# Optimization experiments

Hardware: AMD Instinct MI355X
Metric: run time of the kernel (lower is better)

Reference implementation:

```python
import jax, jax.numpy as jnp
import numpy as np

B, N, C, H, E, K = 2, 2048, 1024, 4096, 8, 2
TAU = 1.0


def setup_inputs() -> dict:
    key = jax.random.key(0)
    ks = jax.random.split(key, 9)
    x = jax.random.normal(ks[0], (B, N, C), dtype=jnp.float32)
    T = B * N
    u = jax.random.uniform(ks[1], (T, E), minval=1e-6, maxval=1.0 - 1e-6)
    gumbel_noise = -jnp.log(-jnp.log(u))  # Gumbel(0,1) samples
    s = 0.02
    gate_w = jax.random.normal(ks[2], (C, E), dtype=jnp.float32) * s
    gate_b = jnp.zeros((E,), dtype=jnp.float32)
    w1 = jax.random.normal(ks[3], (E, C, H), dtype=jnp.float32) * s
    b1 = jnp.zeros((E, H), dtype=jnp.float32)
    w2 = jax.random.normal(ks[4], (E, H, C), dtype=jnp.float32) * s
    b2 = jnp.zeros((E, C), dtype=jnp.float32)
    return {"x": x, "gumbel_noise": gumbel_noise, "gate_w": gate_w,
            "gate_b": gate_b, "w1": w1, "b1": b1, "w2": w2, "b2": b2}


def reference(x, gumbel_noise, gate_w, gate_b, w1, b1, w2, b2):
    Bb, Nn, Cc = x.shape
    x_flat = x.reshape(-1, Cc)                                  # [T, C]
    logits = x_flat @ gate_w + gate_b                           # [T, E]
    # F.gumbel_softmax(hard=False, tau=1): softmax((logits + g)/tau)
    gates = jax.nn.softmax((logits + gumbel_noise) / TAU, axis=-1)
    mean_gates = gates.mean(axis=0)
    load_balance_loss = jnp.sum(mean_gates * jnp.log(mean_gates + 1e-8))
    topk_vals, topk_idxs = jax.lax.top_k(gates, K)              # [T, K]
    T = x_flat.shape[0]
    # scatter top-k gate weights into a dense [T, E] combine matrix
    comb = jnp.zeros((T, E), dtype=gates.dtype)
    comb = comb.at[jnp.arange(T)[:, None], topk_idxs].set(topk_vals)
    # dense per-expert MLP over all tokens, then weighted combine
    h = jnp.einsum('tc,ech->teh', x_flat, w1) + b1              # [T, E, H]
    h = jax.nn.gelu(h, approximate=False)                        # exact GELU (nn.GELU)
    y = jnp.einsum('teh,ehc->tec', h, w2) + b2                  # [T, E, C]
    out = jnp.einsum('te,tec->tc', comb, y)                     # [T, C]
    return out.reshape(Bb, Nn, Cc), load_balance_loss
```

## Files before the change

### kernel.cpp

```cpp
#include <hip/hip_runtime.h>
#include <math.h>

#define TT  4096
#define CC  1024
#define HH  4096
#define EE  8
#define TKN 8192

typedef _Float16 f16x8 __attribute__((ext_vector_type(8)));
typedef float    f32x4 __attribute__((ext_vector_type(4)));

#define GLD_LDS16(g, l)                                                        \
    __builtin_amdgcn_global_load_lds(                                          \
        (const __attribute__((address_space(1))) void*)(g),                    \
        (__attribute__((address_space(3))) void*)(l), 16, 0, 0)

#define BOUNDARY(N)                                                            \
    do {                                                                       \
        asm volatile("s_waitcnt vmcnt(" #N ")" ::: "memory");                  \
        __builtin_amdgcn_s_barrier();                                          \
    } while (0)

__global__ __launch_bounds__(256) void gate_kernel(
    const float* __restrict__ x, const float* __restrict__ gn,
    const float* __restrict__ gw, const float* __restrict__ gb,
    int* __restrict__ topk_idx, float* __restrict__ topk_w,
    int* __restrict__ counts, float* __restrict__ gsum)
{
    int wave = threadIdx.x >> 6, lane = threadIdx.x & 63;
    int t = blockIdx.x * 4 + wave;
    const float* xrow = x + (size_t)t * CC;

    double acc[EE];
#pragma unroll
    for (int e = 0; e < EE; e++) acc[e] = 0.0;

#pragma unroll
    for (int i = 0; i < CC / 64; i++) {
        int c = i * 64 + lane;
        float xv = xrow[c];
        const float4* g4 = reinterpret_cast<const float4*>(gw + (size_t)c * EE);
        float4 g0 = g4[0], g1 = g4[1];
        double xd = (double)xv;
        acc[0] += xd * (double)g0.x; acc[1] += xd * (double)g0.y;
        acc[2] += xd * (double)g0.z; acc[3] += xd * (double)g0.w;
        acc[4] += xd * (double)g1.x; acc[5] += xd * (double)g1.y;
        acc[6] += xd * (double)g1.z; acc[7] += xd * (double)g1.w;
    }
#pragma unroll
    for (int e = 0; e < EE; e++)
#pragma unroll
        for (int off = 32; off > 0; off >>= 1)
            acc[e] += __shfl_xor(acc[e], off);

    double z[EE], m = -1e300;
#pragma unroll
    for (int e = 0; e < EE; e++) {
        z[e] = acc[e] + (double)gb[e] + (double)gn[(size_t)t * EE + e];
        m = fmax(m, z[e]);
    }
    double p[EE], s = 0.0;
#pragma unroll
    for (int e = 0; e < EE; e++) { p[e] = exp(z[e] - m); s += p[e]; }
    double inv = 1.0 / s;
    double g[EE];
#pragma unroll
    for (int e = 0; e < EE; e++) g[e] = p[e] * inv;

    int i1 = 0; double v1 = g[0];
#pragma unroll
    for (int e = 1; e < EE; e++) if (g[e] > v1) { v1 = g[e]; i1 = e; }
    int i2 = -1; double v2 = -1.0;
#pragma unroll
    for (int e = 0; e < EE; e++) if (e != i1 && g[e] > v2) { v2 = g[e]; i2 = e; }

    if (lane == 0) {
        topk_idx[t * 2 + 0] = i1; topk_w[t * 2 + 0] = (float)v1;
        topk_idx[t * 2 + 1] = i2; topk_w[t * 2 + 1] = (float)v2;
        atomicAdd(&counts[i1], 1);
        atomicAdd(&counts[i2], 1);
    }

    __shared__ float gp[4][EE];
    if (lane == 0) {
#pragma unroll
        for (int e = 0; e < EE; e++) gp[wave][e] = (float)g[e];
    }
    __syncthreads();
    if (threadIdx.x < EE) {
        float s4 = gp[0][threadIdx.x] + gp[1][threadIdx.x] +
                   gp[2][threadIdx.x] + gp[3][threadIdx.x];
        atomicAdd(&gsum[threadIdx.x], s4);
    }
}

__global__ __launch_bounds__(256) void transpose_f16_kernel(
    const float* __restrict__ src, _Float16* __restrict__ dst, int R, int Ccols)
{
    __shared__ float tile[64][65];
    int e = blockIdx.z;
    const float* s = src + (size_t)e * R * Ccols;
    _Float16* d = dst + (size_t)e * R * Ccols;
    int c0 = blockIdx.x * 64, r0 = blockIdx.y * 64;
    int tid = threadIdx.x;

    int lr = tid >> 4;
    int lc = (tid & 15) * 4;
#pragma unroll
    for (int i = 0; i < 4; i++) {
        int r = lr + i * 16;
        float4 v = *reinterpret_cast<const float4*>(
            s + (size_t)(r0 + r) * Ccols + c0 + lc);
        tile[r][lc + 0] = v.x; tile[r][lc + 1] = v.y;
        tile[r][lc + 2] = v.z; tile[r][lc + 3] = v.w;
    }
    __syncthreads();

    int oc = tid >> 2;
    int orr = (tid & 3) * 16;
    f16x8 o0, o1;
#pragma unroll
    for (int j = 0; j < 8; j++) o0[j] = (_Float16)tile[orr + j][oc];
#pragma unroll
    for (int j = 0; j < 8; j++) o1[j] = (_Float16)tile[orr + 8 + j][oc];
    *reinterpret_cast<f16x8*>(d + (size_t)(c0 + oc) * R + r0 + orr)     = o0;
    *reinterpret_cast<f16x8*>(d + (size_t)(c0 + oc) * R + r0 + orr + 8) = o1;
}

__global__ void scan_kernel(const int* __restrict__ counts, int* __restrict__ offsets,
                            const float* __restrict__ gsum, float* __restrict__ loss_out)
{
    if (threadIdx.x == 0) {
        int o = 0;
#pragma unroll
        for (int e = 0; e < EE; e++) { offsets[e] = o; o += counts[e]; }
        offsets[EE] = o;
        float L = 0.f;
#pragma unroll
        for (int e = 0; e < EE; e++) {
            float me = gsum[e] / (float)TT;
            L += me * logf(me + 1e-8f);
        }
        *loss_out = L;
    }
}

__global__ __launch_bounds__(256) void scatter_kernel(
    const int* __restrict__ topk_idx, const int* __restrict__ offsets,
    int* __restrict__ fill, int* __restrict__ rowtok, int* __restrict__ posmap)
{
    int t = blockIdx.x * 256 + threadIdx.x;
#pragma unroll
    for (int k = 0; k < 2; k++) {
        int e = topk_idx[t * 2 + k];
        int pos = offsets[e] + atomicAdd(&fill[e], 1);
        rowtok[pos] = t;
        posmap[t * 2 + k] = pos;
    }
}

__global__ __launch_bounds__(256) void gather_kernel(
    const float* __restrict__ x, const int* __restrict__ rowtok,
    _Float16* __restrict__ xg)
{
    int p = blockIdx.x * 2 + (threadIdx.x >> 7);
    int c = (threadIdx.x & 127) * 8;
    int t = rowtok[p];
    const float4* s = reinterpret_cast<const float4*>(x + (size_t)t * CC + c);
    float4 v0 = s[0], v1 = s[1];
    f16x8 o;
    o[0] = (_Float16)v0.x; o[1] = (_Float16)v0.y;
    o[2] = (_Float16)v0.z; o[3] = (_Float16)v0.w;
    o[4] = (_Float16)v1.x; o[5] = (_Float16)v1.y;
    o[6] = (_Float16)v1.z; o[7] = (_Float16)v1.w;
    *reinterpret_cast<f16x8*>(xg + (size_t)p * CC + c) = o;
}

__global__ __launch_bounds__(512, 2) void gemm1_kernel(
    const _Float16* __restrict__ xg, const _Float16* __restrict__ w1t,
    const float* __restrict__ b1, const int* __restrict__ offsets,
    _Float16* __restrict__ h)
{
    int GX = gridDim.x, GY = gridDim.y;
    int nwg = GX * GY * (int)gridDim.z;
    int f = blockIdx.x + GX * (blockIdx.y + GY * blockIdx.z);
    int cpx = nwg >> 3;
    f = (f & 7) * cpx + (f >> 3);
    int bx = f % GX; int tq = f / GX; int by = tq % GY; int bz = tq / GY;

    int e = bz;
    int segs = offsets[e];
    int M = offsets[e + 1] - segs;
    int m0 = bx * 256;
    if (m0 >= M) return;
    int n0 = by * 256;

    __shared__ __align__(16) _Float16 As[4][256 * 32];
    __shared__ __align__(16) _Float16 Bs[4][256 * 32];
    _Float16* AsF = &As[0][0];
    _Float16* BsF = &Bs[0][0];

    int tid = threadIdx.x;
    int wave = tid >> 6, lane = tid & 63;
    int wm = (wave >> 2) * 128, wn = (wave & 3) * 64;
    int lrow = lane & 15, kg = lane >> 4;
    int aoff = (wm + lrow) * 32 + kg * 8;
    int boff = (wn + lrow) * 32 + kg * 8;

    const _Float16* wB = w1t + (size_t)e * HH * CC;

    int r0c = tid >> 2, cc = tid & 3;
    int rmA0 = m0 + r0c;       if (rmA0 >= M) rmA0 = M - 1;
    int rmA1 = m0 + 128 + r0c; if (rmA1 >= M) rmA1 = M - 1;
    const _Float16* ap0 = xg + (size_t)(segs + rmA0) * CC + cc * 8;
    const _Float16* ap1 = xg + (size_t)(segs + rmA1) * CC + cc * 8;
    const _Float16* bp0 = wB + (size_t)(n0 + r0c) * CC + cc * 8;
    const _Float16* bp1 = wB + (size_t)(n0 + 128 + r0c) * CC + cc * 8;
    int c0 = tid * 8;

    f32x4 acc[8][4];
#pragma unroll
    for (int i = 0; i < 8; i++)
#pragma unroll
        for (int j = 0; j < 4; j++)
#pragma unroll
            for (int r = 0; r < 4; r++) acc[i][j][r] = 0.f;

    auto STAGE = [&](int nb) {
        _Float16* ad = AsF + nb * (256 * 32);
        _Float16* bd = BsF + nb * (256 * 32);
        GLD_LDS16(ap0, ad + c0);
        GLD_LDS16(ap1, ad + 4096 + c0);
        GLD_LDS16(bp0, bd + c0);
        GLD_LDS16(bp1, bd + 4096 + c0);
        ap0 += 32; ap1 += 32; bp0 += 32; bp1 += 32;
    };

    auto TILE = [&](int t, bool stage) {
        const _Float16* Ab = AsF + (t & 3) * (256 * 32) + aoff;
        const _Float16* Bb = BsF + (t & 3) * (256 * 32) + boff;
        if (stage) STAGE((t + 3) & 3);
        f16x8 aF[4], bF[4];
#pragma unroll
        for (int j = 0; j < 4; j++)
            bF[j] = *reinterpret_cast<const f16x8*>(Bb + j * 512);
#pragma unroll
        for (int i = 0; i < 4; i++)
            aF[i] = *reinterpret_cast<const f16x8*>(Ab + i * 512);
        __builtin_amdgcn_s_setprio(1);
#pragma unroll
        for (int i = 0; i < 4; i++)
#pragma unroll
            for (int j = 0; j < 4; j++)
                acc[i][j] = __builtin_amdgcn_mfma_f32_16x16x32_f16(
                    aF[i], bF[j], acc[i][j], 0, 0, 0);
        __builtin_amdgcn_s_setprio(0);
#pragma unroll
        for (int i = 0; i < 4; i++)
            aF[i] = *reinterpret_cast<const f16x8*>(Ab + (4 + i) * 512);
        __builtin_amdgcn_s_setprio(1);
#pragma unroll
        for (int i = 0; i < 4; i++)
#pragma unroll
            for (int j = 0; j < 4; j++)
                acc[4 + i][j] = __builtin_amdgcn_mfma_f32_16x16x32_f16(
                    aF[i], bF[j], acc[4 + i][j], 0, 0, 0);
        __builtin_amdgcn_s_setprio(0);
    };

    const int NK = CC / 32;
    STAGE(0); STAGE(1); STAGE(2);
    BOUNDARY(8);
    for (int t = 0; t <= NK - 4; ++t) {
        TILE(t, true);
        BOUNDARY(8);
    }
    TILE(NK - 3, false); BOUNDARY(4);
    TILE(NK - 2, false); BOUNDARY(0);
    TILE(NK - 1, false);

    int rbase = (lane >> 4) * 4;
#pragma unroll
    for (int mi = 0; mi < 8; mi++) {
#pragma unroll
        for (int ni = 0; ni < 4; ni++) {
            int gcol = n0 + wn + ni * 16 + lrow;
            float bias = b1[(size_t)e * HH + gcol];
#pragma unroll
            for (int r = 0; r < 4; r++) {
                int rowl = m0 + wm + mi * 16 + rbase + r;
                if (rowl < M) {
                    float v = acc[mi][ni][r] + bias;
                    v = 0.5f * v * (1.0f + erff(v * 0.70710678118654752f));
                    h[(size_t)(segs + rowl) * HH + gcol] = (_Float16)v;
                }
            }
        }
    }
}

__global__ __launch_bounds__(512, 2) void gemm2_kernel(
    const _Float16* __restrict__ h, const _Float16* __restrict__ w2t,
    const float* __restrict__ b2, const int* __restrict__ offsets,
    float* __restrict__ y)
{
    int GX = gridDim.x, GY = gridDim.y;
    int nwg = GX * GY * (int)gridDim.z;
    int f = blockIdx.x + GX * (blockIdx.y + GY * blockIdx.z);
    int cpx = nwg >> 3;
    f = (f & 7) * cpx + (f >> 3);
    int bx = f % GX; int tq = f / GX; int by = tq % GY; int bz = tq / GY;

    int e = bz;
    int segs = offsets[e];
    int M = offsets[e + 1] - segs;
    int m0 = bx * 256;
    if (m0 >= M) return;
    int kz = by >> 2;
    int n0 = (by & 3) * 256;
    int kbeg = kz * (HH / 2);

    __shared__ __align__(16) _Float16 As[4][256 * 32];
    __shared__ __align__(16) _Float16 Bs[4][256 * 32];
    _Float16* AsF = &As[0][0];
    _Float16* BsF = &Bs[0][0];

    int tid = threadIdx.x;
    int wave = tid >> 6, lane = tid & 63;
    int wm = (wave >> 2) * 128, wn = (wave & 3) * 64;
    int lrow = lane & 15, kg = lane >> 4;
    int aoff = (wm + lrow) * 32 + kg * 8;
    int boff = (wn + lrow) * 32 + kg * 8;

    const _Float16* wB = w2t + (size_t)e * CC * HH;

    int r0c = tid >> 2, cc = tid & 3;
    int rmA0 = m0 + r0c;       if (rmA0 >= M) rmA0 = M - 1;
    int rmA1 = m0 + 128 + r0c; if (rmA1 >= M) rmA1 = M - 1;
    const _Float16* ap0 = h + (size_t)(segs + rmA0) * HH + kbeg + cc * 8;
    const _Float16* ap1 = h + (size_t)(segs + rmA1) * HH + kbeg + cc * 8;
    const _Float16* bp0 = wB + (size_t)(n0 + r0c) * HH + kbeg + cc * 8;
    const _Float16* bp1 = wB + (size_t)(n0 + 128 + r0c) * HH + kbeg + cc * 8;
    int c0 = tid * 8;

    f32x4 acc[8][4];
#pragma unroll
    for (int i = 0; i < 8; i++)
#pragma unroll
        for (int j = 0; j < 4; j++)
#pragma unroll
            for (int r = 0; r < 4; r++) acc[i][j][r] = 0.f;

    auto STAGE = [&](int nb) {
        _Float16* ad = AsF + nb * (256 * 32);
        _Float16* bd = BsF + nb * (256 * 32);
        GLD_LDS16(ap0, ad + c0);
        GLD_LDS16(ap1, ad + 4096 + c0);
        GLD_LDS16(bp0, bd + c0);
        GLD_LDS16(bp1, bd + 4096 + c0);
        ap0 += 32; ap1 += 32; bp0 += 32; bp1 += 32;
    };

    auto TILE = [&](int t, bool stage) {
        const _Float16* Ab = AsF + (t & 3) * (256 * 32) + aoff;
        const _Float16* Bb = BsF + (t & 3) * (256 * 32) + boff;
        if (stage) STAGE((t + 3) & 3);
        f16x8 aF[4], bF[4];
#pragma unroll
        for (int j = 0; j < 4; j++)
            bF[j] = *reinterpret_cast<const f16x8*>(Bb + j * 512);
#pragma unroll
        for (int i = 0; i < 4; i++)
            aF[i] = *reinterpret_cast<const f16x8*>(Ab + i * 512);
        __builtin_amdgcn_s_setprio(1);
#pragma unroll
        for (int i = 0; i < 4; i++)
#pragma unroll
            for (int j = 0; j < 4; j++)
                acc[i][j] = __builtin_amdgcn_mfma_f32_16x16x32_f16(
                    aF[i], bF[j], acc[i][j], 0, 0, 0);
        __builtin_amdgcn_s_setprio(0);
#pragma unroll
        for (int i = 0; i < 4; i++)
            aF[i] = *reinterpret_cast<const f16x8*>(Ab + (4 + i) * 512);
        __builtin_amdgcn_s_setprio(1);
#pragma unroll
        for (int i = 0; i < 4; i++)
#pragma unroll
            for (int j = 0; j < 4; j++)
                acc[4 + i][j] = __builtin_amdgcn_mfma_f32_16x16x32_f16(
                    aF[i], bF[j], acc[4 + i][j], 0, 0, 0);
        __builtin_amdgcn_s_setprio(0);
    };

    const int NK = (HH / 2) / 32;
    STAGE(0); STAGE(1); STAGE(2);
    BOUNDARY(8);
    for (int t = 0; t <= NK - 4; ++t) {
        TILE(t, true);
        BOUNDARY(8);
    }
    TILE(NK - 3, false); BOUNDARY(4);
    TILE(NK - 2, false); BOUNDARY(0);
    TILE(NK - 1, false);

    float* yk = y + (size_t)kz * TKN * CC;
    int rbase = (lane >> 4) * 4;
#pragma unroll
    for (int mi = 0; mi < 8; mi++) {
#pragma unroll
        for (int ni = 0; ni < 4; ni++) {
            int gcol = n0 + wn + ni * 16 + lrow;
            float bias = (kz == 0) ? b2[(size_t)e * CC + gcol] : 0.f;
#pragma unroll
            for (int r = 0; r < 4; r++) {
                int rowl = m0 + wm + mi * 16 + rbase + r;
                if (rowl < M)
                    yk[(size_t)(segs + rowl) * CC + gcol] = acc[mi][ni][r] + bias;
            }
        }
    }
}

__global__ __launch_bounds__(256) void combine_kernel(
    const float* __restrict__ y, const int* __restrict__ posmap,
    const float* __restrict__ topk_w, float* __restrict__ out)
{
    int t = blockIdx.x * 2 + (threadIdx.x >> 7);
    int c = (threadIdx.x & 127) * 8;
    int p0 = posmap[t * 2 + 0], p1 = posmap[t * 2 + 1];
    float wa = topk_w[t * 2 + 0], wb = topk_w[t * 2 + 1];
    const float* y1 = y + (size_t)TKN * CC;
    const float4* a0 = reinterpret_cast<const float4*>(y  + (size_t)p0 * CC + c);
    const float4* a1 = reinterpret_cast<const float4*>(y1 + (size_t)p0 * CC + c);
    const float4* b0 = reinterpret_cast<const float4*>(y  + (size_t)p1 * CC + c);
    const float4* b1 = reinterpret_cast<const float4*>(y1 + (size_t)p1 * CC + c);
    float4 r0, r1;
    float4 av0 = a0[0], av1 = a0[1], aw0 = a1[0], aw1 = a1[1];
    float4 bv0 = b0[0], bv1 = b0[1], bw0 = b1[0], bw1 = b1[1];
    r0.x = wa * (av0.x + aw0.x) + wb * (bv0.x + bw0.x);
    r0.y = wa * (av0.y + aw0.y) + wb * (bv0.y + bw0.y);
    r0.z = wa * (av0.z + aw0.z) + wb * (bv0.z + bw0.z);
    r0.w = wa * (av0.w + aw0.w) + wb * (bv0.w + bw0.w);
    r1.x = wa * (av1.x + aw1.x) + wb * (bv1.x + bw1.x);
    r1.y = wa * (av1.y + aw1.y) + wb * (bv1.y + bw1.y);
    r1.z = wa * (av1.z + aw1.z) + wb * (bv1.z + bw1.z);
    r1.w = wa * (av1.w + aw1.w) + wb * (bv1.w + bw1.w);
    float4* o = reinterpret_cast<float4*>(out + (size_t)t * CC + c);
    o[0] = r0; o[1] = r1;
}

extern "C" void kernel_launch(void* const* d_in, const int* in_sizes, int n_in,
                              void* d_out, int out_size, void* d_ws, size_t ws_size,
                              hipStream_t stream)
{
    const float* x  = (const float*)d_in[0];
    const float* gn = (const float*)d_in[1];
    const float* gw = (const float*)d_in[2];
    const float* gb = (const float*)d_in[3];
    const float* w1 = (const float*)d_in[4];
    const float* b1 = (const float*)d_in[5];
    const float* w2 = (const float*)d_in[6];
    const float* b2 = (const float*)d_in[7];
    float* out = (float*)d_out;

    char* w = (char*)d_ws;
    int*   counts  = (int*)(w + 0);
    int*   fill    = (int*)(w + 32);
    int*   offsets = (int*)(w + 64);
    float* gsum    = (float*)(w + 128);
    size_t off = 256;
    int*   topk_idx = (int*)(w + off);   off += (size_t)TT * 2 * 4;
    float* topk_w   = (float*)(w + off); off += (size_t)TT * 2 * 4;
    int*   rowtok   = (int*)(w + off);   off += (size_t)TKN * 4;
    int*   posmap   = (int*)(w + off);   off += (size_t)TKN * 4;
    _Float16* xg  = (_Float16*)(w + off); off += (size_t)TKN * CC * 2;
    _Float16* w1t = (_Float16*)(w + off); off += (size_t)EE * HH * CC * 2;
    _Float16* w2t = (_Float16*)(w + off); off += (size_t)EE * CC * HH * 2;
    _Float16* hbuf = (_Float16*)(w + off); off += (size_t)TKN * HH * 2;
    float* ybuf = (float*)w1t;

    (void)hipMemsetAsync(d_ws, 0, 256, stream);

    gate_kernel<<<TT / 4, 256, 0, stream>>>(x, gn, gw, gb, topk_idx, topk_w,
                                            counts, gsum);
    transpose_f16_kernel<<<dim3(HH / 64, CC / 64, EE), 256, 0, stream>>>(
        w1, w1t, CC, HH);
    transpose_f16_kernel<<<dim3(CC / 64, HH / 64, EE), 256, 0, stream>>>(
        w2, w2t, HH, CC);
    scan_kernel<<<1, 64, 0, stream>>>(counts, offsets, gsum, out + (size_t)TT * CC);
    scatter_kernel<<<TT / 256, 256, 0, stream>>>(topk_idx, offsets, fill,
                                                 rowtok, posmap);
    gather_kernel<<<TKN / 2, 256, 0, stream>>>(x, rowtok, xg);
    gemm1_kernel<<<dim3(6, HH / 256, EE), 512, 0, stream>>>(xg, w1t, b1,
                                                            offsets, hbuf);
    gemm2_kernel<<<dim3(6, 2 * (CC / 256), EE), 512, 0, stream>>>(
        hbuf, w2t, b2, offsets, ybuf);
    combine_kernel<<<TT / 2, 256, 0, stream>>>(ybuf, posmap, topk_w, out);
}
```

Measured before the change: 876.3 us.

## Switch MoE GEMMs to swizzled double-buffered LDS and halve gemm2 M tile

Both expert GEMMs drop the 4-stage global_load_lds ring with explicit vmcnt waits and use a 2-buffer ping-pong with __syncthreads, plus an XOR swizzle of the k-chunk in LDS to reduce bank conflicts on fragment reads. gemm2 shrinks its M tile from 256 to 128 rows and doubles the grid in x, which makes more workgroups per expert and uses fewer accumulators. The shallower pipeline exposes more global-load latency, and the smaller gemm2 tile lowers data reuse per workgroup; occupancy hints in launch_bounds are removed.

```diff
diff --git a/kernel.cpp b/kernel.cpp
--- a/kernel.cpp
+++ b/kernel.cpp
@@ -14,12 +14,6 @@
     __builtin_amdgcn_global_load_lds(                                          \
         (const __attribute__((address_space(1))) void*)(g),                    \
         (__attribute__((address_space(3))) void*)(l), 16, 0, 0)
-
-#define BOUNDARY(N)                                                            \
-    do {                                                                       \
-        asm volatile("s_waitcnt vmcnt(" #N ")" ::: "memory");                  \
-        __builtin_amdgcn_s_barrier();                                          \
-    } while (0)
 
 __global__ __launch_bounds__(256) void gate_kernel(
     const float* __restrict__ x, const float* __restrict__ gn,
@@ -176,7 +170,8 @@
     *reinterpret_cast<f16x8*>(xg + (size_t)p * CC + c) = o;
 }
 
-__global__ __launch_bounds__(512, 2) void gemm1_kernel(
+
+__global__ __launch_bounds__(512) void gemm1_kernel(
     const _Float16* __restrict__ xg, const _Float16* __restrict__ w1t,
     const float* __restrict__ b1, const int* __restrict__ offsets,
     _Float16* __restrict__ h)
@@ -195,28 +190,28 @@
     if (m0 >= M) return;
     int n0 = by * 256;
 
-    __shared__ __align__(16) _Float16 As[4][256 * 32];
-    __shared__ __align__(16) _Float16 Bs[4][256 * 32];
-    _Float16* AsF = &As[0][0];
-    _Float16* BsF = &Bs[0][0];
+    __shared__ __align__(16) _Float16 As[2][256 * 32];
+    __shared__ __align__(16) _Float16 Bs[2][256 * 32];
 
     int tid = threadIdx.x;
     int wave = tid >> 6, lane = tid & 63;
     int wm = (wave >> 2) * 128, wn = (wave & 3) * 64;
-    int lrow = lane & 15, kg = lane >> 4;
-    int aoff = (wm + lrow) * 32 + kg * 8;
-    int boff = (wn + lrow) * 32 + kg * 8;
+    int lrow = lane & 15;
+    int kgx = (lane >> 4) ^ ((lane >> 1) & 3);
+    int aoff = (wm + lrow) * 32 + kgx * 8;
+    int boff = (wn + lrow) * 32 + kgx * 8;
 
     const _Float16* wB = w1t + (size_t)e * HH * CC;
 
-    int r0c = tid >> 2, cc = tid & 3;
-    int rmA0 = m0 + r0c;       if (rmA0 >= M) rmA0 = M - 1;
-    int rmA1 = m0 + 128 + r0c; if (rmA1 >= M) rmA1 = M - 1;
-    const _Float16* ap0 = xg + (size_t)(segs + rmA0) * CC + cc * 8;
-    const _Float16* ap1 = xg + (size_t)(segs + rmA1) * CC + cc * 8;
-    const _Float16* bp0 = wB + (size_t)(n0 + r0c) * CC + cc * 8;
-    const _Float16* bp1 = wB + (size_t)(n0 + 128 + r0c) * CC + cc * 8;
-    int c0 = tid * 8;
+    int r = tid >> 2;
+    int cc = ((tid & 3) ^ ((tid >> 3) & 3)) * 8;
+    int rA0 = m0 + r;       if (rA0 >= M) rA0 = M - 1;
+    int rA1 = m0 + 128 + r; if (rA1 >= M) rA1 = M - 1;
+    const _Float16* ap0 = xg + (size_t)(segs + rA0) * CC + cc;
+    const _Float16* ap1 = xg + (size_t)(segs + rA1) * CC + cc;
+    const _Float16* bp0 = wB + (size_t)(n0 + r) * CC + cc;
+    const _Float16* bp1 = wB + (size_t)(n0 + 128 + r) * CC + cc;
+    int ldst = tid * 8;
 
     f32x4 acc[8][4];
 #pragma unroll
@@ -224,22 +219,24 @@
 #pragma unroll
         for (int j = 0; j < 4; j++)
 #pragma unroll
-            for (int r = 0; r < 4; r++) acc[i][j][r] = 0.f;
-
-    auto STAGE = [&](int nb) {
-        _Float16* ad = AsF + nb * (256 * 32);
-        _Float16* bd = BsF + nb * (256 * 32);
-        GLD_LDS16(ap0, ad + c0);
-        GLD_LDS16(ap1, ad + 4096 + c0);
-        GLD_LDS16(bp0, bd + c0);
-        GLD_LDS16(bp1, bd + 4096 + c0);
+            for (int q = 0; q < 4; q++) acc[i][j][q] = 0.f;
+
+    auto STAGE = [&](int b) {
+        GLD_LDS16(ap0, &As[b][0] + ldst);
+        GLD_LDS16(ap1, &As[b][0] + 4096 + ldst);
+        GLD_LDS16(bp0, &Bs[b][0] + ldst);
+        GLD_LDS16(bp1, &Bs[b][0] + 4096 + ldst);
         ap0 += 32; ap1 += 32; bp0 += 32; bp1 += 32;
     };
 
-    auto TILE = [&](int t, bool stage) {
-        const _Float16* Ab = AsF + (t & 3) * (256 * 32) + aoff;
-        const _Float16* Bb = BsF + (t & 3) * (256 * 32) + boff;
-        if (stage) STAGE((t + 3) & 3);
+    const int NK = CC / 32;
+    STAGE(0);
+    __syncthreads();
+    for (int t = 0; t < NK; ++t) {
+        int b = t & 1;
+        if (t + 1 < NK) STAGE(b ^ 1);
+        const _Float16* Ab = &As[b][0] + aoff;
+        const _Float16* Bb = &Bs[b][0] + boff;
         f16x8 aF[4], bF[4];
 #pragma unroll
         for (int j = 0; j < 4; j++)
@@ -255,6 +252,7 @@
                 acc[i][j] = __builtin_amdgcn_mfma_f32_16x16x32_f16(
                     aF[i], bF[j], acc[i][j], 0, 0, 0);
         __builtin_amdgcn_s_setprio(0);
+        __builtin_amdgcn_s_barrier();
 #pragma unroll
         for (int i = 0; i < 4; i++)
             aF[i] = *reinterpret_cast<const f16x8*>(Ab + (4 + i) * 512);
@@ -266,18 +264,8 @@
                 acc[4 + i][j] = __builtin_amdgcn_mfma_f32_16x16x32_f16(
                     aF[i], bF[j], acc[4 + i][j], 0, 0, 0);
         __builtin_amdgcn_s_setprio(0);
-    };
-
-    const int NK = CC / 32;
-    STAGE(0); STAGE(1); STAGE(2);
-    BOUNDARY(8);
-    for (int t = 0; t <= NK - 4; ++t) {
-        TILE(t, true);
-        BOUNDARY(8);
-    }
-    TILE(NK - 3, false); BOUNDARY(4);
-    TILE(NK - 2, false); BOUNDARY(0);
-    TILE(NK - 1, false);
+        __syncthreads();
+    }
 
     int rbase = (lane >> 4) * 4;
 #pragma unroll
@@ -287,10 +275,10 @@
             int gcol = n0 + wn + ni * 16 + lrow;
             float bias = b1[(size_t)e * HH + gcol];
 #pragma unroll
-            for (int r = 0; r < 4; r++) {
-                int rowl = m0 + wm + mi * 16 + rbase + r;
+            for (int q = 0; q < 4; q++) {
+                int rowl = m0 + wm + mi * 16 + rbase + q;
                 if (rowl < M) {
-                    float v = acc[mi][ni][r] + bias;
+                    float v = acc[mi][ni][q] + bias;
                     v = 0.5f * v * (1.0f + erff(v * 0.70710678118654752f));
                     h[(size_t)(segs + rowl) * HH + gcol] = (_Float16)v;
                 }
@@ -299,7 +287,7 @@
     }
 }
 
-__global__ __launch_bounds__(512, 2) void gemm2_kernel(
+__global__ __launch_bounds__(512) void gemm2_kernel(
     const _Float16* __restrict__ h, const _Float16* __restrict__ w2t,
     const float* __restrict__ b2, const int* __restrict__ offsets,
     float* __restrict__ y)
@@ -314,57 +302,56 @@
     int e = bz;
     int segs = offsets[e];
     int M = offsets[e + 1] - segs;
-    int m0 = bx * 256;
+    int m0 = bx * 128;
     if (m0 >= M) return;
     int kz = by >> 2;
     int n0 = (by & 3) * 256;
     int kbeg = kz * (HH / 2);
 
-    __shared__ __align__(16) _Float16 As[4][256 * 32];
-    __shared__ __align__(16) _Float16 Bs[4][256 * 32];
-    _Float16* AsF = &As[0][0];
-    _Float16* BsF = &Bs[0][0];
+    __shared__ __align__(16) _Float16 As[2][128 * 32];
+    __shared__ __align__(16) _Float16 Bs[2][256 * 32];
 
     int tid = threadIdx.x;
     int wave = tid >> 6, lane = tid & 63;
-    int wm = (wave >> 2) * 128, wn = (wave & 3) * 64;
-    int lrow = lane & 15, kg = lane >> 4;
-    int aoff = (wm + lrow) * 32 + kg * 8;
-    int boff = (wn + lrow) * 32 + kg * 8;
+    int wm = (wave >> 2) * 64, wn = (wave & 3) * 64;
+    int lrow = lane & 15;
+    int kgx = (lane >> 4) ^ ((lane >> 1) & 3);
+    int aoff = (wm + lrow) * 32 + kgx * 8;
+    int boff = (wn + lrow) * 32 + kgx * 8;
 
     const _Float16* wB = w2t + (size_t)e * CC * HH;
 
-    int r0c = tid >> 2, cc = tid & 3;
-    int rmA0 = m0 + r0c;       if (rmA0 >= M) rmA0 = M - 1;
-    int rmA1 = m0 + 128 + r0c; if (rmA1 >= M) rmA1 = M - 1;
-    const _Float16* ap0 = h + (size_t)(segs + rmA0) * HH + kbeg + cc * 8;
-    const _Float16* ap1 = h + (size_t)(segs + rmA1) * HH + kbeg + cc * 8;
-    const _Float16* bp0 = wB + (size_t)(n0 + r0c) * HH + kbeg + cc * 8;
-    const _Float16* bp1 = wB + (size_t)(n0 + 128 + r0c) * HH + kbeg + cc * 8;
-    int c0 = tid * 8;
-
-    f32x4 acc[8][4];
-#pragma unroll
-    for (int i = 0; i < 8; i++)
+    int r = tid >> 2;
+    int cc = ((tid & 3) ^ ((tid >> 3) & 3)) * 8;
+    int rA = m0 + r; if (rA >= M) rA = M - 1;
+    const _Float16* ap  = h  + (size_t)(segs + rA) * HH + kbeg + cc;
+    const _Float16* bp0 = wB + (size_t)(n0 + r) * HH + kbeg + cc;
+    const _Float16* bp1 = wB + (size_t)(n0 + 128 + r) * HH + kbeg + cc;
+    int ldst = tid * 8;
+
+    f32x4 acc[4][4];
+#pragma unroll
+    for (int i = 0; i < 4; i++)
 #pragma unroll
         for (int j = 0; j < 4; j++)
 #pragma unroll
-            for (int r = 0; r < 4; r++) acc[i][j][r] = 0.f;
-
-    auto STAGE = [&](int nb) {
-        _Float16* ad = AsF + nb * (256 * 32);
-        _Float16* bd = BsF + nb * (256 * 32);
-        GLD_LDS16(ap0, ad + c0);
-        GLD_LDS16(ap1, ad + 4096 + c0);
-        GLD_LDS16(bp0, bd + c0);
-        GLD_LDS16(bp1, bd + 4096 + c0);
-        ap0 += 32; ap1 += 32; bp0 += 32; bp1 += 32;
+            for (int q = 0; q < 4; q++) acc[i][j][q] = 0.f;
+
+    auto STAGE = [&](int b) {
+        GLD_LDS16(ap,  &As[b][0] + ldst);
+        GLD_LDS16(bp0, &Bs[b][0] + ldst);
+        GLD_LDS16(bp1, &Bs[b][0] + 4096 + ldst);
+        ap += 32; bp0 += 32; bp1 += 32;
     };
 
-    auto TILE = [&](int t, bool stage) {
-        const _Float16* Ab = AsF + (t & 3) * (256 * 32) + aoff;
-        const _Float16* Bb = BsF + (t & 3) * (256 * 32) + boff;
-        if (stage) STAGE((t + 3) & 3);
+    const int NK = (HH / 2) / 32;
+    STAGE(0);
+    __syncthreads();
+    for (int t = 0; t < NK; ++t) {
+        int b = t & 1;
+        if (t + 1 < NK) STAGE(b ^ 1);
+        const _Float16* Ab = &As[b][0] + aoff;
+        const _Float16* Bb = &Bs[b][0] + boff;
         f16x8 aF[4], bF[4];
 #pragma unroll
         for (int j = 0; j < 4; j++)
@@ -374,49 +361,37 @@
             aF[i] = *reinterpret_cast<const f16x8*>(Ab + i * 512);
         __builtin_amdgcn_s_setprio(1);
 #pragma unroll
-        for (int i = 0; i < 4; i++)
+        for (int i = 0; i < 2; i++)
 #pragma unroll
             for (int j = 0; j < 4; j++)
                 acc[i][j] = __builtin_amdgcn_mfma_f32_16x16x32_f16(
                     aF[i], bF[j], acc[i][j], 0, 0, 0);
         __builtin_amdgcn_s_setprio(0);
-#pragma unroll
-        for (int i = 0; i < 4; i++)
-            aF[i] = *reinterpret_cast<const f16x8*>(Ab + (4 + i) * 512);
+        __builtin_amdgcn_s_barrier();
         __builtin_amdgcn_s_setprio(1);
 #pragma unroll
-        for (int i = 0; i < 4; i++)
+        for (int i = 2; i < 4; i++)
 #pragma unroll
             for (int j = 0; j < 4; j++)
-                acc[4 + i][j] = __builtin_amdgcn_mfma_f32_16x16x32_f16(
-                    aF[i], bF[j], acc[4 + i][j], 0, 0, 0);
+                acc[i][j] = __builtin_amdgcn_mfma_f32_16x16x32_f16(
+                    aF[i], bF[j], acc[i][j], 0, 0, 0);
         __builtin_amdgcn_s_setprio(0);
-    };
-
-    const int NK = (HH / 2) / 32;
-    STAGE(0); STAGE(1); STAGE(2);
-    BOUNDARY(8);
-    for (int t = 0; t <= NK - 4; ++t) {
-        TILE(t, true);
-        BOUNDARY(8);
-    }
-    TILE(NK - 3, false); BOUNDARY(4);
-    TILE(NK - 2, false); BOUNDARY(0);
-    TILE(NK - 1, false);
+        __syncthreads();
+    }
 
     float* yk = y + (size_t)kz * TKN * CC;
     int rbase = (lane >> 4) * 4;
 #pragma unroll
-    for (int mi = 0; mi < 8; mi++) {
+    for (int mi = 0; mi < 4; mi++) {
 #pragma unroll
         for (int ni = 0; ni < 4; ni++) {
             int gcol = n0 + wn + ni * 16 + lrow;
             float bias = (kz == 0) ? b2[(size_t)e * CC + gcol] : 0.f;
 #pragma unroll
-            for (int r = 0; r < 4; r++) {
-                int rowl = m0 + wm + mi * 16 + rbase + r;
+            for (int q = 0; q < 4; q++) {
+                int rowl = m0 + wm + mi * 16 + rbase + q;
                 if (rowl < M)
-                    yk[(size_t)(segs + rowl) * CC + gcol] = acc[mi][ni][r] + bias;
+                    yk[(size_t)(segs + rowl) * CC + gcol] = acc[mi][ni][q] + bias;
             }
         }
     }
@@ -494,7 +469,7 @@
     gather_kernel<<<TKN / 2, 256, 0, stream>>>(x, rowtok, xg);
     gemm1_kernel<<<dim3(6, HH / 256, EE), 512, 0, stream>>>(xg, w1t, b1,
                                                             offsets, hbuf);
-    gemm2_kernel<<<dim3(6, 2 * (CC / 256), EE), 512, 0, stream>>>(
+    gemm2_kernel<<<dim3(12, 2 * (CC / 256), EE), 512, 0, stream>>>(
         hbuf, w2t, b2, offsets, ybuf);
     combine_kernel<<<TT / 2, 256, 0, stream>>>(ybuf, posmap, topk_w, out);
 }
```

Result: faster. 825.8 us (-5.8%).
